# Kernel tuning notes

Measured on AMD Instinct MI355X. Metric: run time of the kernel, lower is better.

Reference implementation:

```python
import jax, jax.numpy as jnp
import numpy as np

N = 50000      # nodes
E = 800000     # edges (avg degree 16)
C_IN = 256
C_OUT = 256
H = 4
D = C_OUT // H  # 64
NEG_SLOPE = 0.2


def setup_inputs() -> dict:
    key = jax.random.key(0)
    ks = jax.random.split(key, 12)
    glorot = lambda k, shape: jax.random.uniform(k, shape, jnp.float32, -1.0, 1.0) * np.sqrt(6.0 / (shape[0] + shape[1]))
    return {
        "x": jax.random.normal(ks[0], (N, C_IN), jnp.float32),
        "src": jax.random.randint(ks[1], (E,), 0, N, jnp.int32),
        "dst": jax.random.randint(ks[2], (E,), 0, N, jnp.int32),
        "Wl": glorot(ks[3], (C_IN, C_OUT)),
        "bl": jnp.zeros((C_OUT,), jnp.float32),
        "Wr": glorot(ks[4], (C_IN, C_OUT)),
        "br": jnp.zeros((C_OUT,), jnp.float32),
        "Wv": glorot(ks[5], (C_IN, C_OUT)),
        "bv": jnp.zeros((C_OUT,), jnp.float32),
        "att_l": jax.random.normal(ks[6], (1, H, D), jnp.float32) * 0.1,
        "att_r": jax.random.normal(ks[7], (1, H, D), jnp.float32) * 0.1,
    }


def reference(x, src, dst, Wl, bl, Wr, br, Wv, bv, att_l, att_r):
    # lambda_policy=None, gcn_mode=False -> lmbda = lmbda2 = 1.0
    n = x.shape[0]
    sl = ((x @ Wl + bl).reshape(n, H, D) * att_l).sum(-1, keepdims=True)  # [N,H,1]
    sr = ((x @ Wr + br).reshape(n, H, D) * att_r).sum(-1, keepdims=True)  # [N,H,1]
    xv = (x @ Wv + bv).reshape(n, H, D)                                    # [N,H,D]

    # --- convolve branch: average scores over in-neighborhood (incl. self) ---
    hlr = jnp.concatenate([sl, sr], axis=1)                   # [N,2H,1]
    conv = jax.ops.segment_sum(hlr[src], dst, num_segments=n)  # sum_{u->v} hsrc[u]
    deg = jax.ops.segment_sum(jnp.ones((src.shape[0],), x.dtype), dst, num_segments=n)
    agg = (hlr + conv) / (1.0 + deg[:, None, None])            # [N,2H,1]
    sl, sr = agg[:, :H], agg[:, H:]

    # --- edge attention: gather-add-leakyrelu, segment softmax over dst ---
    e = jax.nn.leaky_relu(sl[src] + sr[dst], NEG_SLOPE)        # [E,H,1]
    emax = jax.ops.segment_max(e, dst, num_segments=n)
    emax = jnp.where(jnp.isfinite(emax), emax, 0.0)
    ex = jnp.exp(e - emax[dst])
    denom = jax.ops.segment_sum(ex, dst, num_segments=n)
    a = ex / jnp.maximum(denom[dst], 1e-16)                    # [E,H,1]

    # --- weighted message aggregation ---
    out = jax.ops.segment_sum(xv[src] * a, dst, num_segments=n)  # [N,H,D]
    return out
```

## Files before the change

### kernel.cpp

```cpp
#include <hip/hip_runtime.h>

#define C_IN 256
#define C_OUT 256
#define NH 4
#define HD 64
#define NEG_SLOPE 0.2f

typedef _Float16 half8 __attribute__((ext_vector_type(8)));
typedef _Float16 half4v __attribute__((ext_vector_type(4)));
typedef float floatx4 __attribute__((ext_vector_type(4)));

__global__ void make_eff_w(const float* __restrict__ Wl, const float* __restrict__ Wr,
                           const float* __restrict__ bl, const float* __restrict__ br,
                           const float* __restrict__ attl, const float* __restrict__ attr,
                           float* __restrict__ Ws, float* __restrict__ bs)
{
    int c = blockIdx.x;
    int t = threadIdx.x;
    int h = t >> 6, d = t & 63;
    float al = attl[t], ar = attr[t];
    float vl, vr;
    if (c < C_IN) { vl = Wl[c * C_OUT + t] * al; vr = Wr[c * C_OUT + t] * ar; }
    else          { vl = bl[t] * al;             vr = br[t] * ar; }
#pragma unroll
    for (int off = 32; off >= 1; off >>= 1) {
        vl += __shfl_xor(vl, off, 64);
        vr += __shfl_xor(vr, off, 64);
    }
    if (d == 0) {
        if (c < C_IN) { Ws[c * 8 + h] = vl; Ws[c * 8 + 4 + h] = vr; }
        else          { bs[h] = vl;         bs[4 + h] = vr; }
    }
}

__global__ void transpose_w(const float* __restrict__ Wv, _Float16* __restrict__ WvT)
{
    int idx = blockIdx.x * 256 + threadIdx.x;
    int n = idx >> 8, k = idx & 255;
    WvT[n * 256 + k] = (_Float16)Wv[k * 256 + n];
}

__global__ __launch_bounds__(256) void gemm_xv(const float* __restrict__ x,
    const _Float16* __restrict__ WvT, const float* __restrict__ bv,
    const float* __restrict__ Ws, const float* __restrict__ bs,
    _Float16* __restrict__ xv, float* __restrict__ s, int M)
{
    __shared__ __align__(16) _Float16 As[128][40];
    __shared__ __align__(16) _Float16 Bs[128][40];
    int tid = threadIdx.x;
    int wid = tid >> 6, lane = tid & 63;
    int quad = lane >> 4, r16 = lane & 15;
    int m0 = blockIdx.x * 128, n0 = blockIdx.y * 128;
    bool do_s = (blockIdx.y == 0);

    floatx4 acc[2][8];
#pragma unroll
    for (int i = 0; i < 2; ++i)
#pragma unroll
        for (int j = 0; j < 8; ++j) acc[i][j] = (floatx4){0.f, 0.f, 0.f, 0.f};

    int arow = tid >> 3, af4 = tid & 7;
    int brow = tid >> 2, bg  = tid & 3;

    float sacc[4][8];
#pragma unroll
    for (int p = 0; p < 4; ++p)
#pragma unroll
        for (int j = 0; j < 8; ++j) sacc[p][j] = 0.f;

    for (int k0 = 0; k0 < 256; k0 += 32) {
        float w8[4][8];
        if (do_s) {
#pragma unroll
            for (int q = 0; q < 4; ++q) {
                const float4* wr = (const float4*)(Ws + (size_t)(k0 + af4 * 4 + q) * 8);
                float4 wa = wr[0], wb = wr[1];
                w8[q][0] = wa.x; w8[q][1] = wa.y; w8[q][2] = wa.z; w8[q][3] = wa.w;
                w8[q][4] = wb.x; w8[q][5] = wb.y; w8[q][6] = wb.z; w8[q][7] = wb.w;
            }
        }
#pragma unroll
        for (int p = 0; p < 4; ++p) {
            int rr = arow + p * 32;
            int gm = m0 + rr;
            float4 v = make_float4(0.f, 0.f, 0.f, 0.f);
            if (gm < M) v = *(const float4*)(x + (size_t)gm * 256 + k0 + af4 * 4);
            half4v tmp;
            tmp[0] = (_Float16)v.x; tmp[1] = (_Float16)v.y;
            tmp[2] = (_Float16)v.z; tmp[3] = (_Float16)v.w;
            *(half4v*)&As[rr][af4 * 4] = tmp;
            if (do_s) {
                float xq[4] = {v.x, v.y, v.z, v.w};
#pragma unroll
                for (int q = 0; q < 4; ++q)
#pragma unroll
                    for (int j = 0; j < 8; ++j)
                        sacc[p][j] += xq[q] * w8[q][j];
            }
        }
#pragma unroll
        for (int p = 0; p < 2; ++p) {
            int nr = brow + p * 64;
            *(float4*)&Bs[nr][bg * 8] = *(const float4*)(WvT + (size_t)(n0 + nr) * 256 + k0 + bg * 8);
        }
        __syncthreads();
        half8 a[2], b[8];
#pragma unroll
        for (int rg = 0; rg < 2; ++rg)
            a[rg] = *(const half8*)&As[wid * 32 + rg * 16 + r16][quad * 8];
#pragma unroll
        for (int cg = 0; cg < 8; ++cg)
            b[cg] = *(const half8*)&Bs[cg * 16 + r16][quad * 8];
#pragma unroll
        for (int rg = 0; rg < 2; ++rg)
#pragma unroll
            for (int cg = 0; cg < 8; ++cg)
                acc[rg][cg] = __builtin_amdgcn_mfma_f32_16x16x32_f16(a[rg], b[cg], acc[rg][cg], 0, 0, 0);
        __syncthreads();
    }

    if (do_s) {
        float b0[8];
#pragma unroll
        for (int j = 0; j < 8; ++j) b0[j] = bs[j];
#pragma unroll
        for (int p = 0; p < 4; ++p) {
#pragma unroll
            for (int o = 1; o <= 4; o <<= 1)
#pragma unroll
                for (int j = 0; j < 8; ++j)
                    sacc[p][j] += __shfl_xor(sacc[p][j], o, 64);
            int gm = m0 + arow + p * 32;
            if (af4 == 0 && gm < M) {
                *(float4*)(s + (size_t)gm * 8)     = make_float4(sacc[p][0] + b0[0], sacc[p][1] + b0[1], sacc[p][2] + b0[2], sacc[p][3] + b0[3]);
                *(float4*)(s + (size_t)gm * 8 + 4) = make_float4(sacc[p][4] + b0[4], sacc[p][5] + b0[5], sacc[p][6] + b0[6], sacc[p][7] + b0[7]);
            }
        }
    }

#pragma unroll
    for (int rg = 0; rg < 2; ++rg) {
        int rbase = m0 + wid * 32 + rg * 16 + quad * 4;
#pragma unroll
        for (int cg = 0; cg < 8; ++cg) {
            int gcol = n0 + cg * 16 + r16;
            float bias = bv[gcol];
#pragma unroll
            for (int rr = 0; rr < 4; ++rr) {
                int grow = rbase + rr;
                if (grow < M)
                    xv[(size_t)grow * 256 + gcol] = (_Float16)(acc[rg][cg][rr] + bias);
            }
        }
    }
}

__global__ void deg_kernel(const int* __restrict__ dst, int* __restrict__ deg, int E)
{
    int i = blockIdx.x * 256 + threadIdx.x;
    int base = i * 4;
    if (base >= E) return;
    if (base + 4 <= E) {
        int4 d = *(const int4*)(dst + base);
        atomicAdd(&deg[d.x], 1);
        atomicAdd(&deg[d.y], 1);
        atomicAdd(&deg[d.z], 1);
        atomicAdd(&deg[d.w], 1);
    } else {
        for (int k = base; k < E; ++k) atomicAdd(&deg[dst[k]], 1);
    }
}

__global__ void scan_part(const int* __restrict__ deg, int* __restrict__ partials,
                          int N, int chunk)
{
    __shared__ int sd[256];
    int b = blockIdx.x, t = threadIdx.x;
    int idx = b * chunk + t;
    int v = (t < chunk && idx < N) ? deg[idx] : 0;
    sd[t] = v; __syncthreads();
    for (int off = 128; off >= 1; off >>= 1) {
        if (t < off) sd[t] += sd[t + off];
        __syncthreads();
    }
    if (t == 0) partials[b] = sd[0];
}

__global__ void scan_partials(const int* __restrict__ partials, int* __restrict__ pscan)
{
    __shared__ int sd[256];
    int t = threadIdx.x;
    int v = partials[t];
    sd[t] = v; __syncthreads();
    for (int off = 1; off < 256; off <<= 1) {
        int x = (t >= off) ? sd[t - off] : 0;
        __syncthreads();
        sd[t] += x;
        __syncthreads();
    }
    pscan[t] = sd[t] - v;
}

__global__ void scan_final(const int* __restrict__ deg, const int* __restrict__ pscan,
                           int* __restrict__ offs, int N, int chunk)
{
    __shared__ int sd[256];
    int b = blockIdx.x, t = threadIdx.x;
    int idx = b * chunk + t;
    int v = (t < chunk && idx < N) ? deg[idx] : 0;
    sd[t] = v; __syncthreads();
    for (int off = 1; off < 256; off <<= 1) {
        int x = (t >= off) ? sd[t - off] : 0;
        __syncthreads();
        sd[t] += x;
        __syncthreads();
    }
    int incl = sd[t], excl = incl - v;
    int base = pscan[b];
    if (t < chunk && idx < N) offs[idx] = base + excl;
    if (idx == N - 1) offs[N] = base + incl;
}

__global__ void scatter_kernel(const int* __restrict__ src, const int* __restrict__ dst,
                               const int* __restrict__ offs, int* __restrict__ cursor,
                               int* __restrict__ csr_src, int E)
{
    int i = blockIdx.x * 256 + threadIdx.x;
    int base = i * 4;
    if (base >= E) return;
    if (base + 4 <= E) {
        int4 d  = *(const int4*)(dst + base);
        int4 sv = *(const int4*)(src + base);
        int p0 = offs[d.x] + atomicAdd(&cursor[d.x], 1); csr_src[p0] = sv.x;
        int p1 = offs[d.y] + atomicAdd(&cursor[d.y], 1); csr_src[p1] = sv.y;
        int p2 = offs[d.z] + atomicAdd(&cursor[d.z], 1); csr_src[p2] = sv.z;
        int p3 = offs[d.w] + atomicAdd(&cursor[d.w], 1); csr_src[p3] = sv.w;
    } else {
        for (int k = base; k < E; ++k) {
            int d = dst[k];
            int p = offs[d] + atomicAdd(&cursor[d], 1);
            csr_src[p] = src[k];
        }
    }
}

__global__ void agg_kernel(const float* __restrict__ s, const int* __restrict__ csr_src,
                           const int* __restrict__ offs, const int* __restrict__ deg,
                           float* __restrict__ aggl, float* __restrict__ aggr, int N)
{
    int gid = blockIdx.x * 256 + threadIdx.x;
    int n = gid >> 3, c = gid & 7;
    if (n >= N) return;
    int off = offs[n], dg = deg[n];
    float acc = s[(size_t)n * 8 + c];
    int i = 0;
    for (; i + 4 <= dg; i += 4) {
        int p0 = csr_src[off + i];
        int p1 = csr_src[off + i + 1];
        int p2 = csr_src[off + i + 2];
        int p3 = csr_src[off + i + 3];
        float v0 = s[(size_t)p0 * 8 + c];
        float v1 = s[(size_t)p1 * 8 + c];
        float v2 = s[(size_t)p2 * 8 + c];
        float v3 = s[(size_t)p3 * 8 + c];
        acc += (v0 + v1) + (v2 + v3);
    }
    for (; i < dg; ++i) acc += s[(size_t)csr_src[off + i] * 8 + c];
    acc *= 1.0f / (1.0f + (float)dg);
    if (c < 4) aggl[(size_t)n * 4 + c]     = acc;
    else       aggr[(size_t)n * 4 + c - 4] = acc;
}

template<int SZ>
__device__ __forceinline__ void gather_sub(int cs, float w, int base, int grp, int lof,
    const _Float16* __restrict__ xv,
    float& o0, float& o1, float& o2, float& o3)
{
    half4v hv[SZ];
#pragma unroll
    for (int j = 0; j < SZ; ++j) {
        int sidx = __builtin_amdgcn_readlane(cs, base + j);
        hv[j] = *(const half4v*)(xv + (((unsigned)sidx << 8) + lof));
    }
#pragma unroll
    for (int j = 0; j < SZ; ++j) {
        float wv = __shfl(w, grp + base + j, 64);
        o0 += wv * (float)hv[j][0];
        o1 += wv * (float)hv[j][1];
        o2 += wv * (float)hv[j][2];
        o3 += wv * (float)hv[j][3];
    }
}

__device__ __forceinline__ void do_chunk(int cs, float w, int cnt, int grp, int lof,
    const _Float16* __restrict__ xv,
    float& o0, float& o1, float& o2, float& o3)
{
    if (cnt == 16) { gather_sub<16>(cs, w, 0, grp, lof, xv, o0, o1, o2, o3); return; }
    int b = 0;
    if (cnt & 8) { gather_sub<8>(cs, w, b, grp, lof, xv, o0, o1, o2, o3); b += 8; }
    if (cnt & 4) { gather_sub<4>(cs, w, b, grp, lof, xv, o0, o1, o2, o3); b += 4; }
    if (cnt & 2) { gather_sub<2>(cs, w, b, grp, lof, xv, o0, o1, o2, o3); b += 2; }
    if (cnt & 1) { gather_sub<1>(cs, w, b, grp, lof, xv, o0, o1, o2, o3); }
}

__global__ __launch_bounds__(256) void attn_out(const float* __restrict__ aggl,
    const float* __restrict__ aggr, const int* __restrict__ csr_src,
    const int* __restrict__ offs, const int* __restrict__ deg,
    const _Float16* __restrict__ xv, float* __restrict__ out, int N)
{
    int wid = threadIdx.x >> 6, lane = threadIdx.x & 63;
    int n = blockIdx.x * 4 + wid;
    if (n >= N) return;
    int myhead = lane >> 4, myedge = lane & 15, grp = lane & 48;
    int lof = lane << 2;
    int off = offs[n], dg = deg[n];
    const int* cb = csr_src + off;
    float ar = aggr[(unsigned)(n * 4 + myhead)];

    float o0 = 0.f, o1 = 0.f, o2 = 0.f, o3 = 0.f;

    int cs0 = 0, cs1 = 0, cs2 = 0, cs3 = 0;
    int e1 = myedge + 16, e2 = myedge + 32, e3 = myedge + 48;
    if (myedge < dg) cs0 = cb[myedge];
    if (e1 < dg)     cs1 = cb[e1];
    if (e2 < dg)     cs2 = cb[e2];
    if (e3 < dg)     cs3 = cb[e3];
    float a0 = 0.f, a1 = 0.f, a2 = 0.f, a3 = 0.f;
    if (myedge < dg) a0 = aggl[(unsigned)((cs0 << 2) + myhead)];
    if (e1 < dg)     a1 = aggl[(unsigned)((cs1 << 2) + myhead)];
    if (e2 < dg)     a2 = aggl[(unsigned)((cs2 << 2) + myhead)];
    if (e3 < dg)     a3 = aggl[(unsigned)((cs3 << 2) + myhead)];
    float w0 = 0.f, w1 = 0.f, w2 = 0.f, w3 = 0.f;
    if (myedge < dg) { float e = a0 + ar; e = (e > 0.f) ? e : NEG_SLOPE * e; w0 = __expf(e); }
    if (e1 < dg)     { float e = a1 + ar; e = (e > 0.f) ? e : NEG_SLOPE * e; w1 = __expf(e); }
    if (e2 < dg)     { float e = a2 + ar; e = (e > 0.f) ? e : NEG_SLOPE * e; w2 = __expf(e); }
    if (e3 < dg)     { float e = a3 + ar; e = (e > 0.f) ? e : NEG_SLOPE * e; w3 = __expf(e); }
    float denom = w0; denom += w1; denom += w2; denom += w3;

    int c0 = dg < 16 ? dg : 16;
    do_chunk(cs0, w0, c0, grp, lof, xv, o0, o1, o2, o3);
    if (dg > 16) {
        int c1 = dg - 16 < 16 ? dg - 16 : 16;
        do_chunk(cs1, w1, c1, grp, lof, xv, o0, o1, o2, o3);
    }
    if (dg > 32) {
        int c2 = dg - 32 < 16 ? dg - 32 : 16;
        do_chunk(cs2, w2, c2, grp, lof, xv, o0, o1, o2, o3);
    }
    if (dg > 48) {
        int c3 = dg - 48 < 16 ? dg - 48 : 16;
        do_chunk(cs3, w3, c3, grp, lof, xv, o0, o1, o2, o3);
    }
    for (int b = 64; b < dg; b += 16) {
        int cs = 0; float w = 0.f;
        if (b + myedge < dg) {
            cs = cb[b + myedge];
            float e = aggl[(unsigned)((cs << 2) + myhead)] + ar;
            e = (e > 0.f) ? e : NEG_SLOPE * e;
            w = __expf(e);
        }
        denom += w;
        int cnt = dg - b < 16 ? dg - b : 16;
        do_chunk(cs, w, cnt, grp, lof, xv, o0, o1, o2, o3);
    }

#pragma unroll
    for (int o = 1; o <= 8; o <<= 1) denom += __shfl_xor(denom, o, 64);
    float inv = 1.0f / fmaxf(denom, 1e-16f);
    floatx4 res = {o0 * inv, o1 * inv, o2 * inv, o3 * inv};
    __builtin_nontemporal_store(res, (floatx4*)(out + (size_t)n * 256 + lof));
}

extern "C" void kernel_launch(void* const* d_in, const int* in_sizes, int n_in,
                              void* d_out, int out_size, void* d_ws, size_t ws_size,
                              hipStream_t stream)
{
    const float* x    = (const float*)d_in[0];
    const int*   src  = (const int*)d_in[1];
    const int*   dst  = (const int*)d_in[2];
    const float* Wl   = (const float*)d_in[3];
    const float* bl   = (const float*)d_in[4];
    const float* Wr   = (const float*)d_in[5];
    const float* br   = (const float*)d_in[6];
    const float* Wv   = (const float*)d_in[7];
    const float* bv   = (const float*)d_in[8];
    const float* attl = (const float*)d_in[9];
    const float* attr = (const float*)d_in[10];
    float* out = (float*)d_out;

    int N = in_sizes[0] / C_IN;
    int E = in_sizes[1];

    char* p = (char*)d_ws;
    auto alloc = [&](size_t bytes) -> void* {
        uintptr_t q = (uintptr_t)p;
        q = (q + 255) & ~(uintptr_t)255;
        p = (char*)(q + bytes);
        return (void*)q;
    };
    float* Ws     = (float*)alloc((size_t)C_IN * 8 * sizeof(float));
    float* bs     = (float*)alloc(8 * sizeof(float));
    float* s      = (float*)alloc((size_t)N * 8 * sizeof(float));
    float* aggl   = (float*)alloc((size_t)N * 4 * sizeof(float));
    float* aggr   = (float*)alloc((size_t)N * 4 * sizeof(float));
    int* deg      = (int*)alloc((size_t)N * sizeof(int));
    int* offs     = (int*)alloc((size_t)(N + 1) * sizeof(int));
    int* cursor   = (int*)alloc((size_t)N * sizeof(int));
    int* partials = (int*)alloc(256 * sizeof(int));
    int* pscan    = (int*)alloc(256 * sizeof(int));
    int* csr_src  = (int*)alloc((size_t)E * sizeof(int));
    _Float16* WvT = (_Float16*)alloc((size_t)C_IN * C_OUT * sizeof(_Float16));
    _Float16* xv  = (_Float16*)alloc((size_t)N * C_OUT * sizeof(_Float16));

    hipMemsetAsync(deg, 0, (size_t)N * sizeof(int), stream);
    hipMemsetAsync(cursor, 0, (size_t)N * sizeof(int), stream);

    make_eff_w<<<C_IN + 1, 256, 0, stream>>>(Wl, Wr, bl, br, attl, attr, Ws, bs);
    transpose_w<<<(C_IN * C_OUT) / 256, 256, 0, stream>>>(Wv, WvT);
    gemm_xv<<<dim3((N + 127) / 128, C_OUT / 128), 256, 0, stream>>>(x, WvT, bv, Ws, bs, xv, s, N);
    deg_kernel<<<((E + 3) / 4 + 255) / 256, 256, 0, stream>>>(dst, deg, E);
    int chunk = (N + 255) / 256;
    scan_part<<<256, 256, 0, stream>>>(deg, partials, N, chunk);
    scan_partials<<<1, 256, 0, stream>>>(partials, pscan);
    scan_final<<<256, 256, 0, stream>>>(deg, pscan, offs, N, chunk);
    scatter_kernel<<<((E + 3) / 4 + 255) / 256, 256, 0, stream>>>(src, dst, offs, cursor, csr_src, E);
    agg_kernel<<<(N * 8 + 255) / 256, 256, 0, stream>>>(s, csr_src, offs, deg, aggl, aggr, N);
    attn_out<<<(N + 3) / 4, 256, 0, stream>>>(aggl, aggr, csr_src, offs, deg, xv, out, N);
}
```

Measured before the change: 330.8 us.

## Restructure xv GEMM into per-wave 16-row strips without shared memory

The GEMM kernel changes from 128x128 block tiles staged through LDS with barriers to independent waves. Each wave computes a 16-row strip across all 256 output columns, loading A fragments straight from global memory and B fragments straight from the fp16 transposed weight, which stays cache-resident. This reads x once instead of twice (the old grid had two column blocks), removes the __syncthreads, and spreads the attention-score dot product across every wave instead of only the y==0 blocks. In exchange the B tile is no longer shared through LDS, the B loads are strided, and each wave holds 16 accumulators, which raises register pressure and may lower occupancy.

```diff
diff --git a/kernel.cpp b/kernel.cpp
--- a/kernel.cpp
+++ b/kernel.cpp
@@ -45,113 +45,70 @@
     const float* __restrict__ Ws, const float* __restrict__ bs,
     _Float16* __restrict__ xv, float* __restrict__ s, int M)
 {
-    __shared__ __align__(16) _Float16 As[128][40];
-    __shared__ __align__(16) _Float16 Bs[128][40];
-    int tid = threadIdx.x;
-    int wid = tid >> 6, lane = tid & 63;
-    int quad = lane >> 4, r16 = lane & 15;
-    int m0 = blockIdx.x * 128, n0 = blockIdx.y * 128;
-    bool do_s = (blockIdx.y == 0);
-
-    floatx4 acc[2][8];
-#pragma unroll
-    for (int i = 0; i < 2; ++i)
-#pragma unroll
-        for (int j = 0; j < 8; ++j) acc[i][j] = (floatx4){0.f, 0.f, 0.f, 0.f};
-
-    int arow = tid >> 3, af4 = tid & 7;
-    int brow = tid >> 2, bg  = tid & 3;
-
-    float sacc[4][8];
-#pragma unroll
-    for (int p = 0; p < 4; ++p)
-#pragma unroll
-        for (int j = 0; j < 8; ++j) sacc[p][j] = 0.f;
+    int wv   = blockIdx.x * 4 + (threadIdx.x >> 6);
+    int lane = threadIdx.x & 63;
+    int r16 = lane & 15, quad = lane >> 4;
+    int m0 = wv * 16;
+    if (m0 >= M) return;
+
+    int arow = m0 + r16;
+    int arow_c = arow < M ? arow : M - 1;
+    const float* xrow = x + (size_t)arow_c * 256 + quad * 8;
+
+    floatx4 acc[16];
+#pragma unroll
+    for (int cg = 0; cg < 16; ++cg) acc[cg] = (floatx4){0.f, 0.f, 0.f, 0.f};
+    float sacc[8];
+#pragma unroll
+    for (int j = 0; j < 8; ++j) sacc[j] = 0.f;
 
     for (int k0 = 0; k0 < 256; k0 += 32) {
-        float w8[4][8];
-        if (do_s) {
-#pragma unroll
-            for (int q = 0; q < 4; ++q) {
-                const float4* wr = (const float4*)(Ws + (size_t)(k0 + af4 * 4 + q) * 8);
-                float4 wa = wr[0], wb = wr[1];
-                w8[q][0] = wa.x; w8[q][1] = wa.y; w8[q][2] = wa.z; w8[q][3] = wa.w;
-                w8[q][4] = wb.x; w8[q][5] = wb.y; w8[q][6] = wb.z; w8[q][7] = wb.w;
-            }
-        }
-#pragma unroll
-        for (int p = 0; p < 4; ++p) {
-            int rr = arow + p * 32;
-            int gm = m0 + rr;
-            float4 v = make_float4(0.f, 0.f, 0.f, 0.f);
-            if (gm < M) v = *(const float4*)(x + (size_t)gm * 256 + k0 + af4 * 4);
-            half4v tmp;
-            tmp[0] = (_Float16)v.x; tmp[1] = (_Float16)v.y;
-            tmp[2] = (_Float16)v.z; tmp[3] = (_Float16)v.w;
-            *(half4v*)&As[rr][af4 * 4] = tmp;
-            if (do_s) {
-                float xq[4] = {v.x, v.y, v.z, v.w};
-#pragma unroll
-                for (int q = 0; q < 4; ++q)
-#pragma unroll
-                    for (int j = 0; j < 8; ++j)
-                        sacc[p][j] += xq[q] * w8[q][j];
-            }
-        }
-#pragma unroll
-        for (int p = 0; p < 2; ++p) {
-            int nr = brow + p * 64;
-            *(float4*)&Bs[nr][bg * 8] = *(const float4*)(WvT + (size_t)(n0 + nr) * 256 + k0 + bg * 8);
-        }
-        __syncthreads();
-        half8 a[2], b[8];
-#pragma unroll
-        for (int rg = 0; rg < 2; ++rg)
-            a[rg] = *(const half8*)&As[wid * 32 + rg * 16 + r16][quad * 8];
-#pragma unroll
-        for (int cg = 0; cg < 8; ++cg)
-            b[cg] = *(const half8*)&Bs[cg * 16 + r16][quad * 8];
-#pragma unroll
-        for (int rg = 0; rg < 2; ++rg)
-#pragma unroll
-            for (int cg = 0; cg < 8; ++cg)
-                acc[rg][cg] = __builtin_amdgcn_mfma_f32_16x16x32_f16(a[rg], b[cg], acc[rg][cg], 0, 0, 0);
-        __syncthreads();
-    }
-
-    if (do_s) {
-        float b0[8];
-#pragma unroll
-        for (int j = 0; j < 8; ++j) b0[j] = bs[j];
-#pragma unroll
-        for (int p = 0; p < 4; ++p) {
-#pragma unroll
-            for (int o = 1; o <= 4; o <<= 1)
-#pragma unroll
-                for (int j = 0; j < 8; ++j)
-                    sacc[p][j] += __shfl_xor(sacc[p][j], o, 64);
-            int gm = m0 + arow + p * 32;
-            if (af4 == 0 && gm < M) {
-                *(float4*)(s + (size_t)gm * 8)     = make_float4(sacc[p][0] + b0[0], sacc[p][1] + b0[1], sacc[p][2] + b0[2], sacc[p][3] + b0[3]);
-                *(float4*)(s + (size_t)gm * 8 + 4) = make_float4(sacc[p][4] + b0[4], sacc[p][5] + b0[5], sacc[p][6] + b0[6], sacc[p][7] + b0[7]);
-            }
-        }
-    }
-
-#pragma unroll
-    for (int rg = 0; rg < 2; ++rg) {
-        int rbase = m0 + wid * 32 + rg * 16 + quad * 4;
-#pragma unroll
-        for (int cg = 0; cg < 8; ++cg) {
-            int gcol = n0 + cg * 16 + r16;
-            float bias = bv[gcol];
-#pragma unroll
-            for (int rr = 0; rr < 4; ++rr) {
-                int grow = rbase + rr;
-                if (grow < M)
-                    xv[(size_t)grow * 256 + gcol] = (_Float16)(acc[rg][cg][rr] + bias);
-            }
-        }
+        float4 xa = *(const float4*)(xrow + k0);
+        float4 xb = *(const float4*)(xrow + k0 + 4);
+        half8 af;
+        af[0] = (_Float16)xa.x; af[1] = (_Float16)xa.y;
+        af[2] = (_Float16)xa.z; af[3] = (_Float16)xa.w;
+        af[4] = (_Float16)xb.x; af[5] = (_Float16)xb.y;
+        af[6] = (_Float16)xb.z; af[7] = (_Float16)xb.w;
+
+        const float* wsr = Ws + (unsigned)(k0 + quad * 8) * 8;
+        float xf[8] = {xa.x, xa.y, xa.z, xa.w, xb.x, xb.y, xb.z, xb.w};
+#pragma unroll
+        for (int j2 = 0; j2 < 8; ++j2) {
+            float4 wa = *(const float4*)(wsr + j2 * 8);
+            float4 wb = *(const float4*)(wsr + j2 * 8 + 4);
+            sacc[0] += xf[j2] * wa.x; sacc[1] += xf[j2] * wa.y;
+            sacc[2] += xf[j2] * wa.z; sacc[3] += xf[j2] * wa.w;
+            sacc[4] += xf[j2] * wb.x; sacc[5] += xf[j2] * wb.y;
+            sacc[6] += xf[j2] * wb.z; sacc[7] += xf[j2] * wb.w;
+        }
+
+#pragma unroll
+        for (int cg = 0; cg < 16; ++cg) {
+            half8 bf = *(const half8*)(WvT + (unsigned)((cg * 16 + r16) * 256 + k0 + quad * 8));
+            acc[cg] = __builtin_amdgcn_mfma_f32_16x16x32_f16(af, bf, acc[cg], 0, 0, 0);
+        }
+    }
+
+#pragma unroll
+    for (int cg = 0; cg < 16; ++cg) {
+        int gcol = cg * 16 + r16;
+        float bias = bv[gcol];
+#pragma unroll
+        for (int rr = 0; rr < 4; ++rr) {
+            int grow = m0 + quad * 4 + rr;
+            if (grow < M)
+                xv[(size_t)grow * 256 + gcol] = (_Float16)(acc[cg][rr] + bias);
+        }
+    }
+
+#pragma unroll
+    for (int o = 16; o <= 32; o <<= 1)
+#pragma unroll
+        for (int j = 0; j < 8; ++j) sacc[j] += __shfl_xor(sacc[j], o, 64);
+    if (quad == 0 && arow < M) {
+        *(float4*)(s + (size_t)arow * 8)     = make_float4(sacc[0] + bs[0], sacc[1] + bs[1], sacc[2] + bs[2], sacc[3] + bs[3]);
+        *(float4*)(s + (size_t)arow * 8 + 4) = make_float4(sacc[4] + bs[4], sacc[5] + bs[5], sacc[6] + bs[6], sacc[7] + bs[7]);
     }
 }
 
@@ -418,7 +375,8 @@
 
     make_eff_w<<<C_IN + 1, 256, 0, stream>>>(Wl, Wr, bl, br, attl, attr, Ws, bs);
     transpose_w<<<(C_IN * C_OUT) / 256, 256, 0, stream>>>(Wv, WvT);
-    gemm_xv<<<dim3((N + 127) / 128, C_OUT / 128), 256, 0, stream>>>(x, WvT, bv, Ws, bs, xv, s, N);
+    int nstrips = (N + 15) / 16;
+    gemm_xv<<<(nstrips + 3) / 4, 256, 0, stream>>>(x, WvT, bv, Ws, bs, xv, s, N);
     deg_kernel<<<((E + 3) / 4 + 255) / 256, 256, 0, stream>>>(dst, deg, E);
     int chunk = (N + 255) / 256;
     scan_part<<<256, 256, 0, stream>>>(deg, partials, N, chunk);
```

Result: slower. 363.5 us (+9.9%).
